# Optimization experiments

Hardware: AMD Instinct MI355X
Metric: run time of the kernel (lower is better)

The kernel has to match this reference:

```python
import jax, jax.numpy as jnp
import numpy as np
import math

FEATURE_DIM = 1024
NUM_HEADS = 16
HEAD_SIZE = FEATURE_DIM // NUM_HEADS


def setup_inputs() -> dict:
    key = jax.random.key(0)
    ks = jax.random.split(key, 5)
    B, T, C = 4, 2048, FEATURE_DIM
    scale = 1.0 / math.sqrt(C)
    x = jax.random.normal(ks[0], (B, T, C), dtype=jnp.float32)
    # attention_proj: Linear(C, 3C) -> weight (3C, C), bias (3C,)
    W_qkv = jax.random.uniform(ks[1], (3 * C, C), jnp.float32, -scale, scale)
    b_qkv = jax.random.uniform(ks[2], (3 * C,), jnp.float32, -scale, scale)
    # final_proj: Linear(C, C)
    W_out = jax.random.uniform(ks[3], (C, C), jnp.float32, -scale, scale)
    b_out = jax.random.uniform(ks[4], (C,), jnp.float32, -scale, scale)
    return {"x": x, "W_qkv": W_qkv, "b_qkv": b_qkv, "W_out": W_out, "b_out": b_out}


def reference(x, W_qkv, b_qkv, W_out, b_out):
    B, T, C = x.shape
    H, hs = NUM_HEADS, HEAD_SIZE
    qkv = x @ W_qkv.T + b_qkv                     # (B, T, 3C)
    qkv = qkv.reshape(B, T, H, 3 * hs)            # per-head interleaved q|k|v
    q = qkv[..., :hs]                             # (B, T, H, hs)
    k = qkv[..., hs:2 * hs]
    v = qkv[..., 2 * hs:]
    att = jnp.einsum('bthd,bshd->bhts', q, k) / math.sqrt(hs)  # (B, H, T, T)
    att_prob = jax.nn.softmax(att, axis=-1)
    att_v = jnp.einsum('bhts,bshd->bthd', att_prob, v)         # (B, T, H, hs)
    att_v = att_v.reshape(B, T, C)
    return att_v @ W_out.T + b_out
```

## Files before the change

### kernel.cpp

```cpp
#include <hip/hip_runtime.h>
#include <hip/hip_bf16.h>


typedef unsigned short u16;
typedef short bf16x8 __attribute__((ext_vector_type(8)));
typedef float floatx4 __attribute__((ext_vector_type(4)));

#define BB 4
#define TT 2048
#define CC 1024
#define HH 16
#define CEXP 0.18033688f

#if __has_builtin(__builtin_amdgcn_exp2f)
#define EXP2(x) __builtin_amdgcn_exp2f(x)
#else
#define EXP2(x) exp2f(x)
#endif

__device__ __forceinline__ u16 f2bf(float f) {
    __hip_bfloat16 h = __float2bfloat16(f);
    u16 r; __builtin_memcpy(&r, &h, 2); return r;
}
__device__ __forceinline__ unsigned pkbf(float lo, float hi) {
    __hip_bfloat162 h2 = __float22bfloat162_rn(float2{lo, hi});
    unsigned r; __builtin_memcpy(&r, &h2, 4); return r;
}
__device__ __forceinline__ bf16x8 cvt8(const float* p) {
    floatx4 a = *(const floatx4*)p;
    floatx4 b = *(const floatx4*)(p + 4);
    bf16x8 r;
    r[0] = (short)f2bf(a[0]); r[1] = (short)f2bf(a[1]);
    r[2] = (short)f2bf(a[2]); r[3] = (short)f2bf(a[3]);
    r[4] = (short)f2bf(b[0]); r[5] = (short)f2bf(b[1]);
    r[6] = (short)f2bf(b[2]); r[7] = (short)f2bf(b[3]);
    return r;
}
__device__ __forceinline__ int sw8(int row, int slot) {
    return row * 64 + (((slot ^ (row & 7)) & 7) << 3);
}
__device__ __forceinline__ void gll16(const u16* g, u16* l) {
    __builtin_amdgcn_global_load_lds(
        (const __attribute__((address_space(1))) unsigned*)g,
        (__attribute__((address_space(3))) unsigned*)l, 16, 0, 0);
}

__device__ __forceinline__ void pl32swap(unsigned& a, unsigned& b) {
#if __has_builtin(__builtin_amdgcn_permlane32_swap)
    typedef unsigned u32x2 __attribute__((ext_vector_type(2)));
    u32x2 r = __builtin_amdgcn_permlane32_swap(a, b, false, false);
    a = r[0]; b = r[1];
#else
    const bool up = (threadIdx.x & 32) != 0;
    unsigned as = (unsigned)__shfl_xor((int)a, 32);
    unsigned bs = (unsigned)__shfl_xor((int)b, 32);
    unsigned na = up ? bs : a;
    unsigned nb = up ? b : as;
    a = na; b = nb;
#endif
}
__device__ __forceinline__ void pl16swap(unsigned& a, unsigned& b) {
#if __has_builtin(__builtin_amdgcn_permlane16_swap)
    typedef unsigned u32x2 __attribute__((ext_vector_type(2)));
    u32x2 r = __builtin_amdgcn_permlane16_swap(a, b, false, false);
    a = r[0]; b = r[1];
#else
    const bool up = (threadIdx.x & 16) != 0;
    unsigned as = (unsigned)__shfl_xor((int)a, 16);
    unsigned bs = (unsigned)__shfl_xor((int)b, 16);
    unsigned na = up ? bs : a;
    unsigned nb = up ? b : as;
    a = na; b = nb;
#endif
}

__global__ __launch_bounds__(256) void cvt_all(const float* __restrict__ x,
                                               const float* __restrict__ wq,
                                               const float* __restrict__ wo,
                                               u16* __restrict__ xb,
                                               u16* __restrict__ wqb,
                                               u16* __restrict__ wob) {
    const int nx8 = 8388608 / 8, nq8 = 3145728 / 8, no8 = 1048576 / 8;
    const int n8 = nx8 + nq8 + no8;
    for (int i = blockIdx.x * blockDim.x + threadIdx.x; i < n8;
         i += gridDim.x * blockDim.x) {
        const float* src;
        u16* dst;
        if (i < nx8)            { src = x  + (size_t)i * 8;          dst = xb  + (size_t)i * 8; }
        else if (i < nx8 + nq8) { size_t j = i - nx8; src = wq + j * 8; dst = wqb + j * 8; }
        else                    { size_t j = i - nx8 - nq8; src = wo + j * 8; dst = wob + j * 8; }
        floatx4 a = *(const floatx4*)src;
        floatx4 b = *(const floatx4*)(src + 4);
        union { bf16x8 v; unsigned u[4]; } r;
        r.u[0] = pkbf(a[0], a[1]); r.u[1] = pkbf(a[2], a[3]);
        r.u[2] = pkbf(b[0], b[1]); r.u[3] = pkbf(b[2], b[3]);
        *(bf16x8*)dst = r.v;
    }
}

template <int SCATTER, int QSLOT>
__global__ __launch_bounds__(256) void gemm_lds(const u16* __restrict__ Ab,
                                                const u16* __restrict__ Bb,
                                                const float* __restrict__ bias,
                                                void* __restrict__ Cv,
                                                int K, int N) {
    __shared__ u16 As[2][128 * 64];
    __shared__ u16 Bs[2][128 * 64];

    const int tid  = threadIdx.x;
    const int lane = tid & 63;
    const int wave = tid >> 6;
    const int quad = lane >> 4;
    const int l15  = lane & 15;
    const int wm   = (wave >> 1) * 64;
    const int wn   = (wave & 1) * 64;
    const int blockM = blockIdx.y * 128;
    const int blockN = blockIdx.x * 128;

    floatx4 acc[4][4];
#pragma unroll
    for (int i = 0; i < 4; i++)
#pragma unroll
        for (int j = 0; j < 4; j++) acc[i][j] = (floatx4){0.f, 0.f, 0.f, 0.f};

    const int lr = lane >> 3;
    const int scol = ((lane & 7) ^ (lr & 7)) * 8;

    auto stage = [&](int buf, int k0) {
#pragma unroll
        for (int i = 0; i < 4; i++) {
            const int c = wave * 4 + i;
            const int row = blockM + c * 8 + lr;
            const u16* src;
            if (QSLOT) {
                const int b = row >> 11, t = row & 2047, h = k0 >> 6;
                src = Ab + ((size_t)((b * HH + h) * TT + t)) * 192 + scol;
            } else {
                src = Ab + (size_t)row * K + k0 + scol;
            }
            gll16(src, &As[buf][c * 512]);
        }
#pragma unroll
        for (int i = 0; i < 4; i++) {
            const int c = wave * 4 + i;
            const int row = blockN + c * 8 + lr;
            gll16(Bb + (size_t)row * K + k0 + scol, &Bs[buf][c * 512]);
        }
    };

    stage(0, 0);
    __syncthreads();

    int cur = 0;
    for (int k0 = 0; k0 < K; k0 += 64) {
        if (k0 + 64 < K) stage(cur ^ 1, k0 + 64);

#pragma unroll
        for (int ks = 0; ks < 2; ks++) {
            const int slot = ks * 4 + quad;
            bf16x8 af[4], bfr[4];
#pragma unroll
            for (int mi = 0; mi < 4; mi++)
                af[mi] = *(const bf16x8*)&As[cur][sw8(wm + mi * 16 + l15, slot)];
#pragma unroll
            for (int ni = 0; ni < 4; ni++)
                bfr[ni] = *(const bf16x8*)&Bs[cur][sw8(wn + ni * 16 + l15, slot)];
#pragma unroll
            for (int mi = 0; mi < 4; mi++)
#pragma unroll
                for (int ni = 0; ni < 4; ni++)
                    acc[mi][ni] = __builtin_amdgcn_mfma_f32_16x16x32_bf16(
                        af[mi], bfr[ni], acc[mi][ni], 0, 0, 0);
        }

        __syncthreads();
        cur ^= 1;
    }

#pragma unroll
    for (int ni = 0; ni < 4; ni++) {
        const int col = blockN + wn + ni * 16 + l15;
        const float bv = bias[col];
        if (SCATTER) {
            const int h = col / 192;
            const int r = col - h * 192;
            const float qs = (r < 64) ? CEXP : 1.0f;
            u16* C = (u16*)Cv;
#pragma unroll
            for (int mi = 0; mi < 4; mi++)
#pragma unroll
                for (int reg = 0; reg < 4; reg++) {
                    const int row = blockM + wm + mi * 16 + quad * 4 + reg;
                    const int b = row >> 11, t = row & 2047;
                    C[((size_t)((b * HH + h) * TT + t)) * 192 + r] =
                        f2bf((acc[mi][ni][reg] + bv) * qs);
                }
        } else {
            float* C = (float*)Cv;
#pragma unroll
            for (int mi = 0; mi < 4; mi++)
#pragma unroll
                for (int reg = 0; reg < 4; reg++) {
                    const int row = blockM + wm + mi * 16 + quad * 4 + reg;
                    C[(size_t)row * N + col] = acc[mi][ni][reg] + bv;
                }
        }
    }
}

template <int SCATTER, int QSLOT>
__global__ __launch_bounds__(256) void gemm_bt(const void* __restrict__ Av,
                                               const float* __restrict__ Bw,
                                               const float* __restrict__ bias,
                                               void* __restrict__ Cv,
                                               int K, int N) {
    __shared__ u16 As[128 * 64];
    __shared__ u16 Bs[128 * 64];

    const int tid  = threadIdx.x;
    const int lane = tid & 63;
    const int wave = tid >> 6;
    const int quad = lane >> 4;
    const int l15  = lane & 15;
    const int wm   = (wave >> 1) * 64;
    const int wn   = (wave & 1) * 64;
    const int blockM = blockIdx.y * 128;
    const int blockN = blockIdx.x * 128;

    floatx4 acc[4][4];
#pragma unroll
    for (int i = 0; i < 4; i++)
#pragma unroll
        for (int j = 0; j < 4; j++) acc[i][j] = (floatx4){0.f, 0.f, 0.f, 0.f};

    const int srow = lane >> 3;
    const int scol = (lane & 7) * 8;

    for (int k0 = 0; k0 < K; k0 += 64) {
        bf16x8 at[4], bt[4];
#pragma unroll
        for (int i = 0; i < 4; i++) {
            const int row = blockM + (i * 4 + wave) * 8 + srow;
            if (QSLOT) {
                const int b = row >> 11, t = row & 2047, h = k0 >> 6;
                at[i] = *(const bf16x8*)((const u16*)Av
                         + ((size_t)((b * HH + h) * TT + t)) * 192 + scol);
            } else {
                at[i] = cvt8((const float*)Av + (size_t)row * K + k0 + scol);
            }
        }
#pragma unroll
        for (int i = 0; i < 4; i++)
            bt[i] = cvt8(Bw + (size_t)(blockN + (i * 4 + wave) * 8 + srow) * K + k0 + scol);

        __syncthreads();
#pragma unroll
        for (int i = 0; i < 4; i++)
            *(bf16x8*)&As[sw8((i * 4 + wave) * 8 + srow, lane & 7)] = at[i];
#pragma unroll
        for (int i = 0; i < 4; i++)
            *(bf16x8*)&Bs[sw8((i * 4 + wave) * 8 + srow, lane & 7)] = bt[i];
        __syncthreads();

#pragma unroll
        for (int ks = 0; ks < 2; ks++) {
            const int slot = ks * 4 + quad;
            bf16x8 af[4], bfr[4];
#pragma unroll
            for (int mi = 0; mi < 4; mi++)
                af[mi] = *(const bf16x8*)&As[sw8(wm + mi * 16 + l15, slot)];
#pragma unroll
            for (int ni = 0; ni < 4; ni++)
                bfr[ni] = *(const bf16x8*)&Bs[sw8(wn + ni * 16 + l15, slot)];
#pragma unroll
            for (int mi = 0; mi < 4; mi++)
#pragma unroll
                for (int ni = 0; ni < 4; ni++)
                    acc[mi][ni] = __builtin_amdgcn_mfma_f32_16x16x32_bf16(
                        af[mi], bfr[ni], acc[mi][ni], 0, 0, 0);
        }
    }

#pragma unroll
    for (int ni = 0; ni < 4; ni++) {
        const int col = blockN + wn + ni * 16 + l15;
        const float bv = bias[col];
        if (SCATTER) {
            const int h = col / 192;
            const int r = col - h * 192;
            const float qs = (r < 64) ? CEXP : 1.0f;
            u16* C = (u16*)Cv;
#pragma unroll
            for (int mi = 0; mi < 4; mi++)
#pragma unroll
                for (int reg = 0; reg < 4; reg++) {
                    const int row = blockM + wm + mi * 16 + quad * 4 + reg;
                    const int b = row >> 11, t = row & 2047;
                    C[((size_t)((b * HH + h) * TT + t)) * 192 + r] =
                        f2bf((acc[mi][ni][reg] + bv) * qs);
                }
        } else {
            float* C = (float*)Cv;
#pragma unroll
            for (int mi = 0; mi < 4; mi++)
#pragma unroll
                for (int reg = 0; reg < 4; reg++) {
                    const int row = blockM + wm + mi * 16 + quad * 4 + reg;
                    C[(size_t)row * N + col] = acc[mi][ni][reg] + bv;
                }
        }
    }
}

__global__ __launch_bounds__(512) void attn_fwd(u16* __restrict__ qkv) {
    __shared__ u16 Ks[64 * 64];
    __shared__ u16 Vts[64 * 64];

    const int tid  = threadIdx.x;
    const int lane = tid & 63;
    const int wave = tid >> 6;
    const int quad = lane >> 4;
    const int l15  = lane & 15;

    const int bh = blockIdx.y;
    const int t0 = blockIdx.x * 256;
    u16* Qg = qkv + (size_t)bh * TT * 192;

    bf16x8 qf[2][2];
#pragma unroll
    for (int qi = 0; qi < 2; qi++) {
        const int trow = t0 + wave * 32 + qi * 16 + l15;
#pragma unroll
        for (int ks = 0; ks < 2; ks++)
            qf[qi][ks] = *(const bf16x8*)(Qg + (size_t)trow * 192 + ks * 32 + quad * 8);
    }

    bf16x8 ones;
#pragma unroll
    for (int j = 0; j < 8; j++) ones[j] = (short)0x3F80;
    const floatx4 zero4 = (floatx4){0.f, 0.f, 0.f, 0.f};

    floatx4 o[2][4];
#pragma unroll
    for (int qi = 0; qi < 2; qi++)
#pragma unroll
        for (int di = 0; di < 4; di++) o[qi][di] = (floatx4){0.f, 0.f, 0.f, 0.f};
    floatx4 l_acc[2] = {(floatx4){0.f,0.f,0.f,0.f}, (floatx4){0.f,0.f,0.f,0.f}};

    const int lr = lane >> 3;
    const int scolsw = ((lane & 7) ^ (lr & 7)) * 8;
    const int vs  = tid & 63;
    const int vd0 = (tid >> 6) * 8;

    for (int s0 = 0; s0 < TT; s0 += 64) {
        bf16x8 v0 = *(const bf16x8*)(Qg + (size_t)(s0 + vs) * 192 + 128 + vd0);

        __syncthreads();
        gll16(Qg + (size_t)(s0 + wave * 8 + lr) * 192 + 64 + scolsw,
              &Ks[wave * 512]);
        {
            const int vslot = vs >> 3, voff = vs & 7;
#pragma unroll
            for (int j = 0; j < 8; j++) {
                const int row = vd0 + j;
                Vts[row * 64 + (((vslot ^ (row & 7)) & 7) << 3) + voff] = (u16)v0[j];
            }
        }
        __syncthreads();

        floatx4 s_acc[4][2];
        __builtin_amdgcn_s_setprio(1);
        {
            bf16x8 kf[4];
#pragma unroll
            for (int si = 0; si < 4; si++)
                kf[si] = *(const bf16x8*)&Ks[sw8(si * 16 + l15, quad)];
#pragma unroll
            for (int si = 0; si < 4; si++)
#pragma unroll
                for (int qi = 0; qi < 2; qi++)
                    s_acc[si][qi] = __builtin_amdgcn_mfma_f32_16x16x32_bf16(
                        kf[si], qf[qi][0], zero4, 0, 0, 0);
        }
        {
            bf16x8 kf[4];
#pragma unroll
            for (int si = 0; si < 4; si++)
                kf[si] = *(const bf16x8*)&Ks[sw8(si * 16 + l15, 4 + quad)];
#pragma unroll
            for (int si = 0; si < 4; si++)
#pragma unroll
                for (int qi = 0; qi < 2; qi++)
                    s_acc[si][qi] = __builtin_amdgcn_mfma_f32_16x16x32_bf16(
                        kf[si], qf[qi][1], s_acc[si][qi], 0, 0, 0);
        }
        __builtin_amdgcn_s_setprio(0);

        unsigned c[4][2][2];
#pragma unroll
        for (int si = 0; si < 4; si++)
#pragma unroll
            for (int qi = 0; qi < 2; qi++) {
                floatx4 p;
#pragma unroll
                for (int r = 0; r < 4; r++) p[r] = EXP2(s_acc[si][qi][r]);
                c[si][qi][0] = pkbf(p[0], p[1]);
                c[si][qi][1] = pkbf(p[2], p[3]);
            }

        union PF { bf16x8 v; unsigned u[4]; } pf[2][2];
#pragma unroll
        for (int qi = 0; qi < 2; qi++)
#pragma unroll
            for (int ks = 0; ks < 2; ks++)
#pragma unroll
                for (int h = 0; h < 2; h++) {
                    unsigned a = c[2 * ks][qi][h];
                    unsigned b = c[2 * ks + 1][qi][h];
                    pl32swap(a, b);
                    pl16swap(a, b);
                    pf[qi][ks].u[h]     = a;
                    pf[qi][ks].u[2 + h] = b;
                }

        __builtin_amdgcn_s_setprio(1);
#pragma unroll
        for (int ks = 0; ks < 2; ks++) {
            const int slot = ks * 4 + quad;
            bf16x8 vf[4];
#pragma unroll
            for (int di = 0; di < 4; di++)
                vf[di] = *(const bf16x8*)&Vts[sw8(di * 16 + l15, slot)];
#pragma unroll
            for (int qi = 0; qi < 2; qi++) {
#pragma unroll
                for (int di = 0; di < 4; di++)
                    o[qi][di] = __builtin_amdgcn_mfma_f32_16x16x32_bf16(
                        pf[qi][ks].v, vf[di], o[qi][di], 0, 0, 0);
                l_acc[qi] = __builtin_amdgcn_mfma_f32_16x16x32_bf16(
                    pf[qi][ks].v, ones, l_acc[qi], 0, 0, 0);
            }
        }
        __builtin_amdgcn_s_setprio(0);
    }

#pragma unroll
    for (int qi = 0; qi < 2; qi++)
#pragma unroll
        for (int reg = 0; reg < 4; reg++) {
            const float inv_l = 1.0f / l_acc[qi][reg];
            const int trow = t0 + wave * 32 + qi * 16 + quad * 4 + reg;
#pragma unroll
            for (int di = 0; di < 4; di++)
                Qg[(size_t)trow * 192 + di * 16 + l15] = f2bf(o[qi][di][reg] * inv_l);
        }
}

extern "C" void kernel_launch(void* const* d_in, const int* in_sizes, int n_in,
                              void* d_out, int out_size, void* d_ws, size_t ws_size,
                              hipStream_t stream) {
    (void)out_size;
    float* out = (float*)d_out;

    const float *x = nullptr, *wq = nullptr, *bq = nullptr, *wo = nullptr, *bo = nullptr;
    int found = 0;
    for (int i = 0; i < n_in && i < 8; i++) {
        switch (in_sizes[i]) {
            case 8388608: x  = (const float*)d_in[i]; found |= 1;  break;
            case 3145728: wq = (const float*)d_in[i]; found |= 2;  break;
            case 3072:    bq = (const float*)d_in[i]; found |= 4;  break;
            case 1048576: wo = (const float*)d_in[i]; found |= 8;  break;
            case 1024:    bo = (const float*)d_in[i]; found |= 16; break;
        }
    }
    if (found != 31) {
        x  = (const float*)d_in[0]; wq = (const float*)d_in[1];
        bq = (const float*)d_in[2]; wo = (const float*)d_in[3];
        bo = (const float*)d_in[4];
    }

    u16* qkv = (u16*)d_ws;

    const dim3 g1(3 * CC / 128, BB * TT / 128), ga(TT / 256, BB * HH),
               g3(CC / 128, BB * TT / 128);

    if (ws_size >= 75497472u) {
        u16* xb  = qkv + 25165824;
        u16* wqb = qkv + 33554432;
        u16* wob = qkv + 36700160;
        cvt_all<<<2048, 256, 0, stream>>>(x, wq, wo, xb, wqb, wob);
        gemm_lds<1, 0><<<g1, 256, 0, stream>>>(xb, wqb, bq, qkv, CC, 3 * CC);
        attn_fwd<<<ga, 512, 0, stream>>>(qkv);
        gemm_lds<0, 1><<<g3, 256, 0, stream>>>(qkv, wob, bo, out, CC, CC);
    } else {
        gemm_bt<1, 0><<<g1, 256, 0, stream>>>(x, wq, bq, qkv, CC, 3 * CC);
        attn_fwd<<<ga, 512, 0, stream>>>(qkv);
        gemm_bt<0, 1><<<g3, 256, 0, stream>>>(qkv, wo, bo, out, CC, CC);
    }
}
```

Before: 261.8 us.

## Double-buffer K and V tiles in attention loop to overlap loads with MFMA

```diff
diff --git a/kernel.cpp b/kernel.cpp
--- a/kernel.cpp
+++ b/kernel.cpp
@@ -313,8 +313,8 @@
 }
 
 __global__ __launch_bounds__(512) void attn_fwd(u16* __restrict__ qkv) {
-    __shared__ u16 Ks[64 * 64];
-    __shared__ u16 Vts[64 * 64];
+    __shared__ u16 Ks[2][64 * 64];
+    __shared__ u16 Vts[2][64 * 64];
 
     const int tid  = threadIdx.x;
     const int lane = tid & 63;
@@ -351,22 +351,29 @@
     const int scolsw = ((lane & 7) ^ (lr & 7)) * 8;
     const int vs  = tid & 63;
     const int vd0 = (tid >> 6) * 8;
-
+    const int vslot = vs >> 3, voff = vs & 7;
+
+    {
+        bf16x8 v0 = *(const bf16x8*)(Qg + (size_t)vs * 192 + 128 + vd0);
+        gll16(Qg + (size_t)(wave * 8 + lr) * 192 + 64 + scolsw, &Ks[0][wave * 512]);
+#pragma unroll
+        for (int j = 0; j < 8; j++) {
+            const int row = vd0 + j;
+            Vts[0][row * 64 + (((vslot ^ (row & 7)) & 7) << 3) + voff] = (u16)v0[j];
+        }
+    }
+    __syncthreads();
+
+    int cur = 0;
     for (int s0 = 0; s0 < TT; s0 += 64) {
-        bf16x8 v0 = *(const bf16x8*)(Qg + (size_t)(s0 + vs) * 192 + 128 + vd0);
-
-        __syncthreads();
-        gll16(Qg + (size_t)(s0 + wave * 8 + lr) * 192 + 64 + scolsw,
-              &Ks[wave * 512]);
-        {
-            const int vslot = vs >> 3, voff = vs & 7;
-#pragma unroll
-            for (int j = 0; j < 8; j++) {
-                const int row = vd0 + j;
-                Vts[row * 64 + (((vslot ^ (row & 7)) & 7) << 3) + voff] = (u16)v0[j];
-            }
-        }
-        __syncthreads();
+        const int nxt = cur ^ 1;
+        const bool have_next = (s0 + 64 < TT);
+        bf16x8 v_n;
+        if (have_next) {
+            v_n = *(const bf16x8*)(Qg + (size_t)(s0 + 64 + vs) * 192 + 128 + vd0);
+            gll16(Qg + (size_t)(s0 + 64 + wave * 8 + lr) * 192 + 64 + scolsw,
+                  &Ks[nxt][wave * 512]);
+        }
 
         floatx4 s_acc[4][2];
         __builtin_amdgcn_s_setprio(1);
@@ -374,7 +381,7 @@
             bf16x8 kf[4];
 #pragma unroll
             for (int si = 0; si < 4; si++)
-                kf[si] = *(const bf16x8*)&Ks[sw8(si * 16 + l15, quad)];
+                kf[si] = *(const bf16x8*)&Ks[cur][sw8(si * 16 + l15, quad)];
 #pragma unroll
             for (int si = 0; si < 4; si++)
 #pragma unroll
@@ -386,7 +393,7 @@
             bf16x8 kf[4];
 #pragma unroll
             for (int si = 0; si < 4; si++)
-                kf[si] = *(const bf16x8*)&Ks[sw8(si * 16 + l15, 4 + quad)];
+                kf[si] = *(const bf16x8*)&Ks[cur][sw8(si * 16 + l15, 4 + quad)];
 #pragma unroll
             for (int si = 0; si < 4; si++)
 #pragma unroll
@@ -430,7 +437,7 @@
             bf16x8 vf[4];
 #pragma unroll
             for (int di = 0; di < 4; di++)
-                vf[di] = *(const bf16x8*)&Vts[sw8(di * 16 + l15, slot)];
+                vf[di] = *(const bf16x8*)&Vts[cur][sw8(di * 16 + l15, slot)];
 #pragma unroll
             for (int qi = 0; qi < 2; qi++) {
 #pragma unroll
@@ -442,6 +449,18 @@
             }
         }
         __builtin_amdgcn_s_setprio(0);
+
+        if (have_next) {
+#pragma unroll
+            for (int j = 0; j < 8; j++) {
+                const int row = vd0 + j;
+                Vts[nxt][row * 64 + (((vslot ^ (row & 7)) & 7) << 3) + voff] =
+                    (u16)v_n[j];
+            }
+        }
+
+        __syncthreads();
+        cur = nxt;
     }
 
 #pragma unroll
```

New measurement: 270.0 us. +3.1%, slower.
